# Kernel tuning notes

Hardware: AMD Instinct MI355X
Metric: run time of the kernel (lower is better)

Reference implementation:

```python
import jax, jax.numpy as jnp
import numpy as np

B, SQ, SK, H, DH = 4, 4096, 462, 10, 64  # batch, img tokens, text tokens, heads, head dim


def setup_inputs() -> dict:
    key = jax.random.key(0)
    k1, k2, k3, k4, k5 = jax.random.split(key, 5)
    q = jax.random.normal(k1, (B, SQ, H * DH), dtype=jnp.float32)
    k = jax.random.normal(k2, (B, SK, H * DH), dtype=jnp.float32)
    v = jax.random.normal(k3, (B, SK, H * DH), dtype=jnp.float32)
    # mask_scale = H*W / sum(mask) in the original -> positive, >= 1
    mask_scale = 1.0 + 3.0 * jax.random.uniform(k4, (B, H, SQ, SK), dtype=jnp.float32)
    mask_bool = jax.random.randint(k5, (B, H, SQ, SK), 0, 2).astype(bool)
    # guarantee every query row attends to at least one key (avoid all -inf rows)
    mask_bool = mask_bool.at[..., 0].set(True)
    return {"q": q, "k": k, "v": v, "mask_bool": mask_bool,
            "mask_scale": mask_scale, "heads": H}


def reference(q, k, v, mask_bool, mask_scale, heads):
    b, sq, d = q.shape
    dh = d // heads
    # [b, s, h*dh] -> [b, h, s, dh]
    qh = q.reshape(b, sq, heads, dh).transpose(0, 2, 1, 3)
    kh = k.reshape(b, -1, heads, dh).transpose(0, 2, 1, 3)
    vh = v.reshape(b, -1, heads, dh).transpose(0, 2, 1, 3)
    scale = 1.0 / np.sqrt(dh).astype(np.float32)
    scores = jnp.einsum("bhqd,bhkd->bhqk", qh, kh) * scale
    scores = scores * mask_scale
    scores = jnp.where(mask_bool, scores, -jnp.inf)
    attn = jax.nn.softmax(scores, axis=-1)
    out = jnp.einsum("bhqk,bhkd->bhqd", attn, vh)
    return out.transpose(0, 2, 1, 3).reshape(b, sq, d)
```

## Files before the change

kernel.cpp:

```cpp
#include <hip/hip_runtime.h>

#define B_  4
#define SQ_ 4096
#define SK_ 462
#define H_  10
#define DH_ 64
#define D_  (H_ * DH_)

typedef _Float16 half8 __attribute__((ext_vector_type(8)));
typedef float floatx4 __attribute__((ext_vector_type(4)));

__global__ void detect_mask_fmt(const unsigned int* __restrict__ mb_dw,
                                int* __restrict__ flag) {
  __shared__ int s_float, s_byte;
  if (threadIdx.x == 0) { s_float = 0; s_byte = 0; }
  __syncthreads();
  int fl = 0, by = 0;
  for (int i = threadIdx.x; i < 1024; i += 256) {
    unsigned int x = mb_dw[i];
    if (x > 1u) {
      if (x == 0x3F800000u) fl = 1; else by = 1;
    }
  }
  if (fl) atomicOr(&s_float, 1);
  if (by) atomicOr(&s_byte, 1);
  __syncthreads();
  if (threadIdx.x == 0) flag[0] = s_float ? 2 : (s_byte ? 1 : 0);
}

__global__ __launch_bounds__(256)
void attn_fwd(const float* __restrict__ q, const float* __restrict__ k,
              const float* __restrict__ v, const void* __restrict__ mb,
              const float* __restrict__ msc, float* __restrict__ out,
              const int* __restrict__ flag) {
  __shared__ __align__(16) float    qs[64][65];
  __shared__ __align__(16) _Float16 ks[32][66];
  __shared__ __align__(16) _Float16 vts[64][34];
  __shared__ __align__(16) _Float16 ps[4][16][34];

  const int tid  = threadIdx.x;
  const int wave = tid >> 6;
  const int lane = tid & 63;
  const int l16  = lane & 15;
  const int g4   = lane >> 4;

  const int b  = blockIdx.z;
  const int h  = blockIdx.y;
  const int q0 = blockIdx.x * 64;
  const int fmt = flag[0];

  {
    const float* qbase = q + (size_t)(b * SQ_ + q0) * D_ + h * DH_;
    #pragma unroll
    for (int i = 0; i < 4; ++i) {
      int idx4 = tid + i * 256;
      int row  = idx4 >> 4;
      int d4   = (idx4 & 15) * 4;
      float4 val = *reinterpret_cast<const float4*>(qbase + (size_t)row * D_ + d4);
      qs[row][d4 + 0] = val.x; qs[row][d4 + 1] = val.y;
      qs[row][d4 + 2] = val.z; qs[row][d4 + 3] = val.w;
    }
  }
  __syncthreads();

  half8 aq[2];
  {
    int row = wave * 16 + l16;
    #pragma unroll
    for (int kk = 0; kk < 2; ++kk) {
      int dbase = kk * 32 + g4 * 8;
      #pragma unroll
      for (int j = 0; j < 8; ++j) aq[kk][j] = (_Float16)qs[row][dbase + j];
    }
  }

  floatx4 o_acc[4];
  floatx4 l_acc;
  #pragma unroll
  for (int nt = 0; nt < 4; ++nt)
    #pragma unroll
    for (int r = 0; r < 4; ++r) o_acc[nt][r] = 0.0f;
  #pragma unroll
  for (int r = 0; r < 4; ++r) l_acc[r] = 0.0f;

  float m2[4] = {-1e30f, -1e30f, -1e30f, -1e30f};

  unsigned int rowoff[4];
  #pragma unroll
  for (int r = 0; r < 4; ++r) {
    int qrow = q0 + wave * 16 + g4 * 4 + r;
    rowoff[r] = (unsigned int)((b * H_ + h) * SQ_ + qrow) * SK_;
  }

  half8 ones_f;
  #pragma unroll
  for (int j = 0; j < 8; ++j) ones_f[j] = (_Float16)1.0f;

  const float c2 = 0.18033688011112042f;

  const float* kbase = k + (size_t)(b * SK_) * D_ + h * DH_;
  const float* vbase = v + (size_t)(b * SK_) * D_ + h * DH_;

  const int KT = (SK_ + 31) / 32;
  for (int kt = 0; kt < KT; ++kt) {
    __syncthreads();

    #pragma unroll
    for (int i = 0; i < 2; ++i) {
      int idx4 = tid + i * 256;
      int key  = idx4 >> 4;
      int d4   = (idx4 & 15) * 4;
      int gk   = kt * 32 + key;
      int gkc  = gk < SK_ ? gk : SK_ - 1;
      bool okk = gk < SK_;
      float4 kvv = *reinterpret_cast<const float4*>(kbase + (size_t)gkc * D_ + d4);
      float4 vvv = *reinterpret_cast<const float4*>(vbase + (size_t)gkc * D_ + d4);
      ks[key][d4 + 0] = (_Float16)kvv.x; ks[key][d4 + 1] = (_Float16)kvv.y;
      ks[key][d4 + 2] = (_Float16)kvv.z; ks[key][d4 + 3] = (_Float16)kvv.w;
      vts[d4 + 0][key] = okk ? (_Float16)vvv.x : (_Float16)0.0f;
      vts[d4 + 1][key] = okk ? (_Float16)vvv.y : (_Float16)0.0f;
      vts[d4 + 2][key] = okk ? (_Float16)vvv.z : (_Float16)0.0f;
      vts[d4 + 3][key] = okk ? (_Float16)vvv.w : (_Float16)0.0f;
    }

    float mscv[2][4];
    int   mval[2][4];
    #pragma unroll
    for (int ct = 0; ct < 2; ++ct) {
      #pragma unroll
      for (int r = 0; r < 4; ++r) {
        int col = kt * 32 + ct * 16 + l16;
        int cc  = col < SK_ ? col : SK_ - 1;
        unsigned int idx = rowoff[r] + (unsigned int)cc;
        mscv[ct][r] = msc[idx];
        int mv;
        if (fmt == 1)      mv = ((const unsigned char*)mb)[idx] != 0;
        else if (fmt == 0) mv = ((const int*)mb)[idx] != 0;
        else               mv = ((const float*)mb)[idx] != 0.0f;
        mval[ct][r] = (col < SK_) ? mv : 0;
      }
    }
    __syncthreads();

    floatx4 s[2];
    #pragma unroll
    for (int ct = 0; ct < 2; ++ct)
      #pragma unroll
      for (int r = 0; r < 4; ++r) s[ct][r] = 0.0f;
    #pragma unroll
    for (int ct = 0; ct < 2; ++ct) {
      int key = ct * 16 + l16;
      #pragma unroll
      for (int kk = 0; kk < 2; ++kk) {
        half8 kb;
        int dbase = kk * 32 + g4 * 8;
        #pragma unroll
        for (int j = 0; j < 8; ++j) kb[j] = ks[key][dbase + j];
        s[ct] = __builtin_amdgcn_mfma_f32_16x16x32_f16(aq[kk], kb, s[ct], 0, 0, 0);
      }
    }

    float pv[2][4];
    #pragma unroll
    for (int r = 0; r < 4; ++r) {
      float s0 = s[0][r] * (c2 * mscv[0][r]);
      float s1 = s[1][r] * (c2 * mscv[1][r]);
      s0 = mval[0][r] ? s0 : -1e30f;
      s1 = mval[1][r] ? s1 : -1e30f;
      float mx = fmaxf(s0, s1);
      mx = fmaxf(mx, __shfl_xor(mx, 1));
      mx = fmaxf(mx, __shfl_xor(mx, 2));
      mx = fmaxf(mx, __shfl_xor(mx, 4));
      mx = fmaxf(mx, __shfl_xor(mx, 8));
      float mnew  = fmaxf(m2[r], mx);
      float alpha = exp2f(m2[r] - mnew);
      m2[r] = mnew;
      pv[0][r] = exp2f(s0 - mnew);
      pv[1][r] = exp2f(s1 - mnew);
      l_acc[r] *= alpha;
      #pragma unroll
      for (int nt = 0; nt < 4; ++nt) o_acc[nt][r] *= alpha;
    }

    #pragma unroll
    for (int ct = 0; ct < 2; ++ct)
      #pragma unroll
      for (int r = 0; r < 4; ++r)
        ps[wave][g4 * 4 + r][ct * 16 + l16] = (_Float16)pv[ct][r];
    asm volatile("s_waitcnt lgkmcnt(0)" ::: "memory");
    half8 pa;
    #pragma unroll
    for (int j = 0; j < 8; ++j) pa[j] = ps[wave][l16][g4 * 8 + j];

    #pragma unroll
    for (int nt = 0; nt < 4; ++nt) {
      half8 vb;
      int dim = nt * 16 + l16;
      #pragma unroll
      for (int j = 0; j < 8; ++j) vb[j] = vts[dim][g4 * 8 + j];
      o_acc[nt] = __builtin_amdgcn_mfma_f32_16x16x32_f16(pa, vb, o_acc[nt], 0, 0, 0);
    }
    l_acc = __builtin_amdgcn_mfma_f32_16x16x32_f16(pa, ones_f, l_acc, 0, 0, 0);
  }

  #pragma unroll
  for (int r = 0; r < 4; ++r) {
    float inv = 1.0f / l_acc[r];
    int qrow = q0 + wave * 16 + g4 * 4 + r;
    float* ob = out + (size_t)(b * SQ_ + qrow) * D_ + h * DH_;
    #pragma unroll
    for (int nt = 0; nt < 4; ++nt)
      ob[nt * 16 + l16] = o_acc[nt][r] * inv;
  }
}

extern "C" void kernel_launch(void* const* d_in, const int* in_sizes, int n_in,
                              void* d_out, int out_size, void* d_ws, size_t ws_size,
                              hipStream_t stream) {
  const float* q   = (const float*)d_in[0];
  const float* k   = (const float*)d_in[1];
  const float* v   = (const float*)d_in[2];
  const void*  mb  = d_in[3];
  const float* msc = (const float*)d_in[4];
  float* out = (float*)d_out;
  int*   flg = (int*)d_ws;

  detect_mask_fmt<<<1, 256, 0, stream>>>((const unsigned int*)mb, flg);
  dim3 grid(SQ_ / 64, H_, B_);
  attn_fwd<<<grid, 256, 0, stream>>>(q, k, v, mb, msc, out, flg);
}
```

Before: 782.3 us.

## Double-buffer K/V tiles and prefetch next mask tile in registers

The loop now prefetches the next K/V tile and the next mask/scale values into registers while computing the current tile, then stores them into a second LDS buffer. This leaves one barrier per iteration instead of two. Q is loaded straight from global memory into registers, K and P use MFMA-fragment-friendly LDS layouts so each lane does one vector read, and the rescale of the accumulators is skipped when no row max changed. The costs are higher register pressure, which may lower occupancy, and V reads now gather eight separate halves.

New measurement: 858.3 us. 9.7% more time.

```diff
diff --git a/kernel.cpp b/kernel.cpp
--- a/kernel.cpp
+++ b/kernel.cpp
@@ -6,9 +6,12 @@
 #define H_  10
 #define DH_ 64
 #define D_  (H_ * DH_)
-
-typedef _Float16 half8 __attribute__((ext_vector_type(8)));
-typedef float floatx4 __attribute__((ext_vector_type(4)));
+#define KT_ 15
+
+typedef _Float16 half8  __attribute__((ext_vector_type(8)));
+typedef _Float16 half4v __attribute__((ext_vector_type(4)));
+typedef _Float16 half2v __attribute__((ext_vector_type(2)));
+typedef float    floatx4 __attribute__((ext_vector_type(4)));
 
 __global__ void detect_mask_fmt(const unsigned int* __restrict__ mb_dw,
                                 int* __restrict__ flag) {
@@ -33,10 +36,9 @@
               const float* __restrict__ v, const void* __restrict__ mb,
               const float* __restrict__ msc, float* __restrict__ out,
               const int* __restrict__ flag) {
-  __shared__ __align__(16) float    qs[64][65];
-  __shared__ __align__(16) _Float16 ks[32][66];
-  __shared__ __align__(16) _Float16 vts[64][34];
-  __shared__ __align__(16) _Float16 ps[4][16][34];
+  __shared__ __align__(16) _Float16 ksf[2][2048];
+  __shared__ __align__(16) _Float16 vsf[2][32 * 66];
+  __shared__ __align__(16) _Float16 psf[4][512];
 
   const int tid  = threadIdx.x;
   const int wave = tid >> 6;
@@ -49,30 +51,87 @@
   const int q0 = blockIdx.x * 64;
   const int fmt = flag[0];
 
-  {
-    const float* qbase = q + (size_t)(b * SQ_ + q0) * D_ + h * DH_;
-    #pragma unroll
-    for (int i = 0; i < 4; ++i) {
-      int idx4 = tid + i * 256;
-      int row  = idx4 >> 4;
-      int d4   = (idx4 & 15) * 4;
-      float4 val = *reinterpret_cast<const float4*>(qbase + (size_t)row * D_ + d4);
-      qs[row][d4 + 0] = val.x; qs[row][d4 + 1] = val.y;
-      qs[row][d4 + 2] = val.z; qs[row][d4 + 3] = val.w;
-    }
-  }
-  __syncthreads();
+  const float* kbase = k + (size_t)b * SK_ * D_ + h * DH_;
+  const float* vbase = v + (size_t)b * SK_ * D_ + h * DH_;
+  const unsigned char* mb_b = (const unsigned char*)mb;
+  const int*   mb_i = (const int*)mb;
+  const float* mb_f = (const float*)mb;
+
+  int skey[2], sd4[2], wkf[2], wlw[2], wsub[2];
+  #pragma unroll
+  for (int i = 0; i < 2; ++i) {
+    int idx4 = tid + i * 256;
+    skey[i] = idx4 >> 4;
+    sd4[i]  = (idx4 & 15) * 4;
+    int ct = skey[i] >> 4, kk = sd4[i] >> 5, oct = (sd4[i] & 31) >> 3;
+    wkf[i]  = ct * 2 + kk;
+    wlw[i]  = (skey[i] & 15) + 16 * oct;
+    wsub[i] = sd4[i] & 7;
+  }
 
   half8 aq[2];
   {
-    int row = wave * 16 + l16;
+    const float* qp = q + ((size_t)(b * SQ_) + q0 + wave * 16 + l16) * D_ + h * DH_;
     #pragma unroll
     for (int kk = 0; kk < 2; ++kk) {
-      int dbase = kk * 32 + g4 * 8;
-      #pragma unroll
-      for (int j = 0; j < 8; ++j) aq[kk][j] = (_Float16)qs[row][dbase + j];
-    }
-  }
+      float4 f0 = *(const float4*)(qp + kk * 32 + g4 * 8);
+      float4 f1 = *(const float4*)(qp + kk * 32 + g4 * 8 + 4);
+      aq[kk][0] = (_Float16)f0.x; aq[kk][1] = (_Float16)f0.y;
+      aq[kk][2] = (_Float16)f0.z; aq[kk][3] = (_Float16)f0.w;
+      aq[kk][4] = (_Float16)f1.x; aq[kk][5] = (_Float16)f1.y;
+      aq[kk][6] = (_Float16)f1.z; aq[kk][7] = (_Float16)f1.w;
+    }
+  }
+
+  const unsigned rowbase =
+      (unsigned)((b * H_ + h) * SQ_ + q0 + wave * 16 + g4 * 4) * (unsigned)SK_;
+
+  auto kv_load = [&](int kt, float4* kr, float4* vr, int* ok) {
+    #pragma unroll
+    for (int i = 0; i < 2; ++i) {
+      int gk  = kt * 32 + skey[i];
+      int gkc = gk < SK_ ? gk : SK_ - 1;
+      ok[i]   = gk < SK_;
+      kr[i] = *(const float4*)(kbase + (size_t)gkc * D_ + sd4[i]);
+      vr[i] = *(const float4*)(vbase + (size_t)gkc * D_ + sd4[i]);
+    }
+  };
+
+  auto mask_load = [&](int kt, float* mv, unsigned& mok) {
+    mok = 0u;
+    #pragma unroll
+    for (int ct = 0; ct < 2; ++ct) {
+      int col   = kt * 32 + ct * 16 + l16;
+      int cc    = col < SK_ ? col : SK_ - 1;
+      int valid = col < SK_;
+      #pragma unroll
+      for (int r = 0; r < 4; ++r) {
+        unsigned idx = rowbase + (unsigned)(r * SK_) + (unsigned)cc;
+        mv[ct * 4 + r] = msc[idx];
+        int on;
+        if (fmt == 1)      on = mb_b[idx] != 0;
+        else if (fmt == 0) on = mb_i[idx] != 0;
+        else               on = mb_f[idx] != 0.0f;
+        if (valid && on) mok |= 1u << (ct * 4 + r);
+      }
+    }
+  };
+
+  auto kv_store = [&](int buf, const float4* kr, const float4* vr, const int* ok) {
+    #pragma unroll
+    for (int i = 0; i < 2; ++i) {
+      half4v kh;
+      kh[0] = (_Float16)kr[i].x; kh[1] = (_Float16)kr[i].y;
+      kh[2] = (_Float16)kr[i].z; kh[3] = (_Float16)kr[i].w;
+      *(half4v*)&ksf[buf][(wkf[i] * 64 + wlw[i]) * 8 + wsub[i]] = kh;
+      float fx = ok[i] ? vr[i].x : 0.0f, fy = ok[i] ? vr[i].y : 0.0f;
+      float fz = ok[i] ? vr[i].z : 0.0f, fw = ok[i] ? vr[i].w : 0.0f;
+      half2v v01; v01[0] = (_Float16)fx; v01[1] = (_Float16)fy;
+      half2v v23; v23[0] = (_Float16)fz; v23[1] = (_Float16)fw;
+      *(half2v*)&vsf[buf][skey[i] * 66 + sd4[i]]     = v01;
+      *(half2v*)&vsf[buf][skey[i] * 66 + sd4[i] + 2] = v23;
+    }
+  };
 
   floatx4 o_acc[4];
   floatx4 l_acc;
@@ -82,125 +141,97 @@
     for (int r = 0; r < 4; ++r) o_acc[nt][r] = 0.0f;
   #pragma unroll
   for (int r = 0; r < 4; ++r) l_acc[r] = 0.0f;
-
   float m2[4] = {-1e30f, -1e30f, -1e30f, -1e30f};
 
-  unsigned int rowoff[4];
-  #pragma unroll
-  for (int r = 0; r < 4; ++r) {
-    int qrow = q0 + wave * 16 + g4 * 4 + r;
-    rowoff[r] = (unsigned int)((b * H_ + h) * SQ_ + qrow) * SK_;
-  }
-
   half8 ones_f;
   #pragma unroll
   for (int j = 0; j < 8; ++j) ones_f[j] = (_Float16)1.0f;
 
   const float c2 = 0.18033688011112042f;
 
-  const float* kbase = k + (size_t)(b * SK_) * D_ + h * DH_;
-  const float* vbase = v + (size_t)(b * SK_) * D_ + h * DH_;
-
-  const int KT = (SK_ + 31) / 32;
-  for (int kt = 0; kt < KT; ++kt) {
-    __syncthreads();
-
-    #pragma unroll
-    for (int i = 0; i < 2; ++i) {
-      int idx4 = tid + i * 256;
-      int key  = idx4 >> 4;
-      int d4   = (idx4 & 15) * 4;
-      int gk   = kt * 32 + key;
-      int gkc  = gk < SK_ ? gk : SK_ - 1;
-      bool okk = gk < SK_;
-      float4 kvv = *reinterpret_cast<const float4*>(kbase + (size_t)gkc * D_ + d4);
-      float4 vvv = *reinterpret_cast<const float4*>(vbase + (size_t)gkc * D_ + d4);
-      ks[key][d4 + 0] = (_Float16)kvv.x; ks[key][d4 + 1] = (_Float16)kvv.y;
-      ks[key][d4 + 2] = (_Float16)kvv.z; ks[key][d4 + 3] = (_Float16)kvv.w;
-      vts[d4 + 0][key] = okk ? (_Float16)vvv.x : (_Float16)0.0f;
-      vts[d4 + 1][key] = okk ? (_Float16)vvv.y : (_Float16)0.0f;
-      vts[d4 + 2][key] = okk ? (_Float16)vvv.z : (_Float16)0.0f;
-      vts[d4 + 3][key] = okk ? (_Float16)vvv.w : (_Float16)0.0f;
-    }
-
-    float mscv[2][4];
-    int   mval[2][4];
-    #pragma unroll
-    for (int ct = 0; ct < 2; ++ct) {
-      #pragma unroll
-      for (int r = 0; r < 4; ++r) {
-        int col = kt * 32 + ct * 16 + l16;
-        int cc  = col < SK_ ? col : SK_ - 1;
-        unsigned int idx = rowoff[r] + (unsigned int)cc;
-        mscv[ct][r] = msc[idx];
-        int mv;
-        if (fmt == 1)      mv = ((const unsigned char*)mb)[idx] != 0;
-        else if (fmt == 0) mv = ((const int*)mb)[idx] != 0;
-        else               mv = ((const float*)mb)[idx] != 0.0f;
-        mval[ct][r] = (col < SK_) ? mv : 0;
-      }
-    }
-    __syncthreads();
-
-    floatx4 s[2];
-    #pragma unroll
-    for (int ct = 0; ct < 2; ++ct)
-      #pragma unroll
-      for (int r = 0; r < 4; ++r) s[ct][r] = 0.0f;
-    #pragma unroll
-    for (int ct = 0; ct < 2; ++ct) {
-      int key = ct * 16 + l16;
-      #pragma unroll
-      for (int kk = 0; kk < 2; ++kk) {
-        half8 kb;
-        int dbase = kk * 32 + g4 * 8;
-        #pragma unroll
-        for (int j = 0; j < 8; ++j) kb[j] = ks[key][dbase + j];
-        s[ct] = __builtin_amdgcn_mfma_f32_16x16x32_f16(aq[kk], kb, s[ct], 0, 0, 0);
-      }
-    }
-
-    float pv[2][4];
+  float msc_c[8]; unsigned mok_c;
+  {
+    float4 kr[2], vr[2]; int ok[2];
+    kv_load(0, kr, vr, ok);
+    mask_load(0, msc_c, mok_c);
+    kv_store(0, kr, vr, ok);
+  }
+  asm volatile("s_waitcnt lgkmcnt(0)\n\ts_barrier" ::: "memory");
+
+  for (int kt = 0; kt < KT_; ++kt) {
+    const int buf = kt & 1;
+    const bool hasn = (kt + 1 < KT_);
+    float msc_n[8] = {0, 0, 0, 0, 0, 0, 0, 0};
+    unsigned mok_n = 0;
+    float4 kr[2], vr[2]; int ok[2];
+    if (hasn) {
+      kv_load(kt + 1, kr, vr, ok);
+      mask_load(kt + 1, msc_n, mok_n);
+    }
+
+    floatx4 s0v = {0.f, 0.f, 0.f, 0.f}, s1v = {0.f, 0.f, 0.f, 0.f};
+    #pragma unroll
+    for (int kk = 0; kk < 2; ++kk) {
+      half8 kb0 = *(const half8*)&ksf[buf][((0 * 2 + kk) * 64 + lane) * 8];
+      s0v = __builtin_amdgcn_mfma_f32_16x16x32_f16(aq[kk], kb0, s0v, 0, 0, 0);
+      half8 kb1 = *(const half8*)&ksf[buf][((1 * 2 + kk) * 64 + lane) * 8];
+      s1v = __builtin_amdgcn_mfma_f32_16x16x32_f16(aq[kk], kb1, s1v, 0, 0, 0);
+    }
+
+    float pv[2][4], alpha[4];
     #pragma unroll
     for (int r = 0; r < 4; ++r) {
-      float s0 = s[0][r] * (c2 * mscv[0][r]);
-      float s1 = s[1][r] * (c2 * mscv[1][r]);
-      s0 = mval[0][r] ? s0 : -1e30f;
-      s1 = mval[1][r] ? s1 : -1e30f;
+      float s0 = s0v[r] * (c2 * msc_c[r]);
+      float s1 = s1v[r] * (c2 * msc_c[4 + r]);
+      s0 = ((mok_c >> r) & 1u) ? s0 : -1e30f;
+      s1 = ((mok_c >> (4 + r)) & 1u) ? s1 : -1e30f;
       float mx = fmaxf(s0, s1);
       mx = fmaxf(mx, __shfl_xor(mx, 1));
       mx = fmaxf(mx, __shfl_xor(mx, 2));
       mx = fmaxf(mx, __shfl_xor(mx, 4));
       mx = fmaxf(mx, __shfl_xor(mx, 8));
-      float mnew  = fmaxf(m2[r], mx);
-      float alpha = exp2f(m2[r] - mnew);
+      float mnew = fmaxf(m2[r], mx);
+      alpha[r] = exp2f(m2[r] - mnew);
       m2[r] = mnew;
       pv[0][r] = exp2f(s0 - mnew);
       pv[1][r] = exp2f(s1 - mnew);
-      l_acc[r] *= alpha;
-      #pragma unroll
-      for (int nt = 0; nt < 4; ++nt) o_acc[nt][r] *= alpha;
+    }
+    float aprod = alpha[0] * alpha[1] * alpha[2] * alpha[3];
+    if (__any(aprod != 1.0f)) {
+      #pragma unroll
+      for (int r = 0; r < 4; ++r) {
+        l_acc[r] *= alpha[r];
+        #pragma unroll
+        for (int nt = 0; nt < 4; ++nt) o_acc[nt][r] *= alpha[r];
+      }
     }
 
     #pragma unroll
     for (int ct = 0; ct < 2; ++ct)
       #pragma unroll
       for (int r = 0; r < 4; ++r)
-        ps[wave][g4 * 4 + r][ct * 16 + l16] = (_Float16)pv[ct][r];
+        psf[wave][((g4 * 4 + r) + 16 * (ct * 2 + (l16 >> 3))) * 8 + (l16 & 7)] =
+            (_Float16)pv[ct][r];
     asm volatile("s_waitcnt lgkmcnt(0)" ::: "memory");
-    half8 pa;
-    #pragma unroll
-    for (int j = 0; j < 8; ++j) pa[j] = ps[wave][l16][g4 * 8 + j];
+    half8 pa = *(const half8*)&psf[wave][lane * 8];
 
     #pragma unroll
     for (int nt = 0; nt < 4; ++nt) {
       half8 vb;
-      int dim = nt * 16 + l16;
-      #pragma unroll
-      for (int j = 0; j < 8; ++j) vb[j] = vts[dim][g4 * 8 + j];
+      #pragma unroll
+      for (int j = 0; j < 8; ++j)
+        vb[j] = vsf[buf][(g4 * 8 + j) * 66 + nt * 16 + l16];
       o_acc[nt] = __builtin_amdgcn_mfma_f32_16x16x32_f16(pa, vb, o_acc[nt], 0, 0, 0);
     }
     l_acc = __builtin_amdgcn_mfma_f32_16x16x32_f16(pa, ones_f, l_acc, 0, 0, 0);
+
+    if (hasn) kv_store(buf ^ 1, kr, vr, ok);
+
+    #pragma unroll
+    for (int t = 0; t < 8; ++t) msc_c[t] = msc_n[t];
+    mok_c = mok_n;
+
+    asm volatile("s_waitcnt lgkmcnt(0)\n\ts_barrier" ::: "memory");
   }
 
   #pragma unroll
```
